# Optimization experiments

Hardware: AMD Instinct MI355X
Metric: run time of the kernel (lower is better)

## Reference

```python
import jax, jax.numpy as jnp
import numpy as np

NUM_USER = 50000
NUM_ITEM = 50000
N = NUM_USER + NUM_ITEM
DIM_FEAT = 128
DIM_LATENT = 64
DIM_ID = 64
E = 2_000_000
NUM_LAYER = 3
NEG_SLOPE = 0.01  # torch leaky_relu default


def _xavier(key, shape):
    fan_out, fan_in = shape[0], shape[1]
    std = np.sqrt(2.0 / (fan_in + fan_out)).astype(np.float32)
    return jax.random.normal(key, shape, dtype=jnp.float32) * std


def setup_inputs() -> dict:
    key = jax.random.key(0)
    ks = jax.random.split(key, 40)
    features = jax.random.normal(ks[0], (NUM_ITEM, DIM_FEAT), dtype=jnp.float32)
    edge_index = jax.random.randint(ks[1], (2, E), 0, N, dtype=jnp.int32)
    preference = _xavier(ks[2], (NUM_USER, DIM_LATENT))
    mlp_w = _xavier(ks[3], (DIM_LATENT, DIM_FEAT))
    mlp_b = jnp.zeros((DIM_LATENT,), jnp.float32)
    conv_in = [DIM_LATENT, DIM_ID, DIM_ID, DIM_ID, DIM_ID]
    lin_in = [DIM_LATENT, DIM_ID, DIM_ID, DIM_ID, DIM_ID]
    conv_w, lin_w, lin_b, g_w, g_b = [], [], [], [], []
    for i in range(5):
        conv_w.append(_xavier(ks[4 + i], (conv_in[i], DIM_ID)))        # BaseModel weight [in,out]
        lin_w.append(_xavier(ks[9 + i], (DIM_ID, lin_in[i])))           # nn.Linear weight [out,in]
        lin_b.append(jnp.zeros((DIM_ID,), jnp.float32))
        g_w.append(_xavier(ks[14 + i], (DIM_ID, 2 * DIM_ID)))           # concate=True -> in = 2*dim_id
        g_b.append(jnp.zeros((DIM_ID,), jnp.float32))
    return {"features": features, "edge_index": edge_index, "preference": preference,
            "mlp_w": mlp_w, "mlp_b": mlp_b, "conv_w": conv_w,
            "lin_w": lin_w, "lin_b": lin_b, "g_w": g_w, "g_b": g_b}


def reference(features, edge_index, preference, mlp_w, mlp_b, conv_w, lin_w, lin_b, g_w, g_b):
    leaky = lambda x: jax.nn.leaky_relu(x, NEG_SLOPE)
    src, dst = edge_index[0], edge_index[1]

    def conv(x, W):
        # BaseModel: transform then gather at src, scatter-add at dst (aggr='add')
        m = x @ W                                  # [N, dim_id]
        return jax.ops.segment_sum(m[src], dst, num_segments=N)

    temp = features @ mlp_w.T + mlp_b             # MLP (dim_latent branch)
    x = jnp.concatenate([preference, temp], axis=0)  # [N, dim_latent]
    x = x / jnp.maximum(jnp.linalg.norm(x, axis=1, keepdims=True), 1e-12)  # F.normalize

    for i in range(NUM_LAYER):  # layers 1..3 (num_layer=3)
        h = leaky(conv(x, conv_w[i]))
        x_hat = leaky(x @ lin_w[i].T + lin_b[i])
        x = leaky(jnp.concatenate([h, x_hat], axis=1) @ g_w[i].T + g_b[i])

    mu = leaky(conv(x, conv_w[3]))
    x_hat = leaky(x @ lin_w[3].T + lin_b[3])
    mu = jnp.concatenate([mu, x_hat], axis=1) @ g_w[3].T + g_b[3]

    logvar = leaky(conv(x, conv_w[4]))
    x_hat = leaky(x @ lin_w[4].T + lin_b[4])
    logvar = jnp.concatenate([logvar, x_hat], axis=1) @ g_w[4].T + g_b[4]
    return mu, logvar
```

## Files before the change

### kernel.cpp

```cpp
#include <hip/hip_runtime.h>
#include <hip/hip_fp16.h>

#define DEVINL __device__ __forceinline__

typedef _Float16 v4h __attribute__((ext_vector_type(4)));
typedef float    v4f __attribute__((ext_vector_type(4)));

constexpr int NUSER = 50000;
constexpr int NITEM = 50000;
constexpr int NTOT  = 100000;
constexpr int DF    = 128;
constexpr int D     = 64;
constexpr int NE    = 2000000;
constexpr int TR    = 32;
constexpr int ROWH  = 72;
constexpr int NCHUNK = 4;
constexpr int CSPAN  = NTOT / NCHUNK;
constexpr int CCAP   = 32;
constexpr int CAP    = NCHUNK * CCAP;
constexpr int NW     = 512;
constexpr int NPW    = 196;
constexpr int WCAP   = 4608;
constexpr int PBLK   = 512;
constexpr int EPB    = (NE + PBLK - 1) / PBLK;
constexpr int EPT    = (EPB + 255) / 256;

DEVINL float leaky(float v) { return v > 0.f ? v : 0.01f * v; }

DEVINL float2 h2f2(unsigned u) {
  __half2 h = *reinterpret_cast<__half2*>(&u);
  return __half22float2(h);
}

__global__ __launch_bounds__(256) void k_zero(int* __restrict__ p, int n) {
  int i = blockIdx.x * blockDim.x + threadIdx.x;
  if (i < n) p[i] = 0;
}

__global__ __launch_bounds__(256) void k_init_user(
    const float* __restrict__ pref, __half* __restrict__ x16) {
  int wid  = (blockIdx.x * blockDim.x + threadIdx.x) >> 6;
  int lane = threadIdx.x & 63;
  if (wid >= NUSER) return;
  float v = pref[(size_t)wid * D + lane];
  float ss = v * v;
#pragma unroll
  for (int o = 32; o; o >>= 1) ss += __shfl_xor(ss, o);
  float inv = 1.0f / fmaxf(sqrtf(ss), 1e-12f);
  x16[(size_t)wid * D + lane] = __float2half(v * inv);
}

__global__ __launch_bounds__(512) void k_init_item(
    const float* __restrict__ feat, const float* __restrict__ mlp_w,
    const float* __restrict__ mlp_b, __half* __restrict__ x16) {
  __shared__ float sF[TR * DF];
  __shared__ float sP[2][TR][D];
  int tid  = threadIdx.x;
  int lane = tid & 63;
  int wv   = tid >> 6;
  int kh   = wv & 1;
  int rg   = wv >> 1;
  float wh[D];
  const float4* wp = (const float4*)(mlp_w + (size_t)lane * DF + kh * D);
#pragma unroll
  for (int k = 0; k < D / 4; ++k) {
    float4 t = wp[k];
    wh[4 * k] = t.x; wh[4 * k + 1] = t.y; wh[4 * k + 2] = t.z; wh[4 * k + 3] = t.w;
  }
  float bias = mlp_b[lane];
  int t = blockIdx.x;
  {
    const float4* base = (const float4*)(feat + (size_t)t * TR * DF);
    float4* dstl = (float4*)sF;
#pragma unroll
    for (int s = 0; s < 2; ++s) {
      int slot = tid + s * 512;
      int gr = t * TR + (slot >> 5);
      float4 v = make_float4(0.f, 0.f, 0.f, 0.f);
      if (gr < NITEM) v = base[slot];
      dstl[slot] = v;
    }
  }
  __syncthreads();
#pragma unroll
  for (int rr = 0; rr < 8; ++rr) {
    int r = rg * 8 + rr;
    const float4* fr = (const float4*)&sF[r * DF + kh * D];
    float acc = 0.f;
#pragma unroll
    for (int k = 0; k < D / 4; ++k) {
      float4 a = fr[k];
      acc += a.x * wh[4 * k] + a.y * wh[4 * k + 1] + a.z * wh[4 * k + 2] + a.w * wh[4 * k + 3];
    }
    sP[kh][r][lane] = acc;
  }
  __syncthreads();
#pragma unroll
  for (int rr = 0; rr < 4; ++rr) {
    int r = wv * 4 + rr;
    int gr = t * TR + r;
    float v = sP[0][r][lane] + sP[1][r][lane] + bias;
    float ss = v * v;
#pragma unroll
    for (int o = 32; o; o >>= 1) ss += __shfl_xor(ss, o);
    float inv = 1.0f / fmaxf(sqrtf(ss), 1e-12f);
    if (gr < NITEM) x16[(size_t)(NUSER + gr) * D + lane] = __float2half(v * inv);
  }
}

__global__ __launch_bounds__(256) void k_part(
    const int* __restrict__ src, const int* __restrict__ dst,
    int* __restrict__ wcur, unsigned* __restrict__ part) {
  __shared__ int hcnt[NW];
  __shared__ int sc[NW];
  __shared__ int gbase[NW];
  __shared__ int hcur[NW];
  __shared__ unsigned buf[EPB];
  int tid = threadIdx.x;
  int e0 = blockIdx.x * EPB, e1 = min(NE, e0 + EPB);
  for (int i = tid; i < NW; i += 256) { hcnt[i] = 0; hcur[i] = 0; }
  __syncthreads();
  unsigned ent[EPT];
  int wid[EPT];
#pragma unroll
  for (int i = 0; i < EPT; ++i) {
    int e = e0 + tid + i * 256;
    int w = -1; unsigned v = 0;
    if (e < e1) {
      int d = dst[e];
      int s = src[e];
      w = d / NPW;
      v = ((unsigned)(d - w * NPW) << 17) | (unsigned)s;
      atomicAdd(&hcnt[w], 1);
    }
    ent[i] = v; wid[i] = w;
  }
  __syncthreads();
  {
    int i0 = tid, i1 = tid + 256;
    sc[i0] = hcnt[i0]; sc[i1] = hcnt[i1];
    __syncthreads();
    for (int o = 1; o < NW; o <<= 1) {
      int v0 = (i0 >= o) ? sc[i0 - o] : 0;
      int v1 = (i1 >= o) ? sc[i1 - o] : 0;
      __syncthreads();
      sc[i0] += v0; sc[i1] += v1;
      __syncthreads();
    }
  }
  for (int i = tid; i < NW; i += 256)
    gbase[i] = atomicAdd(&wcur[i], hcnt[i]);
  __syncthreads();
#pragma unroll
  for (int i = 0; i < EPT; ++i) {
    int w = wid[i];
    if (w >= 0) {
      int idx = atomicAdd(&hcur[w], 1);
      buf[sc[w] - hcnt[w] + idx] = ent[i];
    }
  }
  __syncthreads();
  int wvv = tid >> 6, lane = tid & 63;
  for (int b = wvv; b < NW; b += 4) {
    int len = hcnt[b];
    int lb = sc[b] - len;
    int gb = gbase[b];
    unsigned* out = part + (size_t)b * WCAP;
    for (int i = lane; i < len; i += 64)
      if (gb + i < WCAP) out[gb + i] = buf[lb + i];
  }
}

__global__ __launch_bounds__(256) void k_scatter_lds(
    const unsigned* __restrict__ part, const int* __restrict__ wcur,
    int* __restrict__ cursor, unsigned short* __restrict__ csr) {
  __shared__ unsigned short lbuck[NPW * CAP];
  __shared__ int lcur[NPW * NCHUNK];
  int tid = threadIdx.x;
  int w   = blockIdx.x;
  int nlo = w * NPW;
  int nn  = min(NPW, NTOT - nlo);
  if (nn <= 0) return;
  for (int i = tid; i < NPW * NCHUNK; i += 256) lcur[i] = 0;
  __syncthreads();
  int cnt = min(wcur[w], WCAP);
  const unsigned* basep = part + (size_t)w * WCAP;
  for (int e = tid; e < cnt; e += 256) {
    unsigned v = basep[e];
    int dl = (int)(v >> 17);
    int s  = (int)(v & 0x1ffffu);
    int c  = s / CSPAN;
    int p  = atomicAdd(&lcur[dl * NCHUNK + c], 1);
    if (p < CCAP) lbuck[dl * CAP + c * CCAP + p] = (unsigned short)(s - c * CSPAN);
  }
  __syncthreads();
  unsigned* gcsr = (unsigned*)(csr + (size_t)nlo * CAP);
  const unsigned* lsrc = (const unsigned*)lbuck;
  int words = nn * (CAP / 2);
  for (int i = tid; i < words; i += 256) gcsr[i] = lsrc[i];
  int* gcur = cursor + (size_t)nlo * NCHUNK;
  for (int i = tid; i < nn * NCHUNK; i += 256) gcur[i] = lcur[i];
}

__global__ __launch_bounds__(256) void k_agg(
    const __half* __restrict__ x16, const int* __restrict__ cnt,
    const unsigned short* __restrict__ csr, __half* __restrict__ agg16) {
  int wid  = (blockIdx.x * blockDim.x + threadIdx.x) >> 6;
  int lane = threadIdx.x & 63;
  if (wid >= NTOT) return;
  int g = lane >> 3;
  int q = lane & 7;
  int4 c4 = *(const int4*)(cnt + ((size_t)wid << 2));
  unsigned w = ((const unsigned*)(csr + (size_t)wid * CAP))[lane];
  float a[8] = {0.f, 0.f, 0.f, 0.f, 0.f, 0.f, 0.f, 0.f};
#pragma unroll
  for (int c = 0; c < NCHUNK; ++c) {
    int deg = min(c == 0 ? c4.x : c == 1 ? c4.y : c == 2 ? c4.z : c4.w, CCAP);
    int base = c * CSPAN;
    int e = 0;
    for (; e + 8 <= deg; e += 8) {
      unsigned u = __shfl(w, c * 16 + ((e + g) >> 1));
      int s = base + (int)((u >> (((e + g) & 1) * 16)) & 0xffffu);
      uint4 v = ((const uint4*)(x16 + (size_t)s * D))[q];
      float2 t;
      t = h2f2(v.x); a[0] += t.x; a[1] += t.y;
      t = h2f2(v.y); a[2] += t.x; a[3] += t.y;
      t = h2f2(v.z); a[4] += t.x; a[5] += t.y;
      t = h2f2(v.w); a[6] += t.x; a[7] += t.y;
    }
    int rem = deg - e;
    if (rem > 0) {
      unsigned u = __shfl(w, c * 16 + ((e + g) >> 1));
      if (g < rem) {
        int s = base + (int)((u >> (((e + g) & 1) * 16)) & 0xffffu);
        uint4 v = ((const uint4*)(x16 + (size_t)s * D))[q];
        float2 t;
        t = h2f2(v.x); a[0] += t.x; a[1] += t.y;
        t = h2f2(v.y); a[2] += t.x; a[3] += t.y;
        t = h2f2(v.z); a[4] += t.x; a[5] += t.y;
        t = h2f2(v.w); a[6] += t.x; a[7] += t.y;
      }
    }
  }
#pragma unroll
  for (int o = 8; o <= 32; o <<= 1) {
#pragma unroll
    for (int i = 0; i < 8; ++i) a[i] += __shfl_xor(a[i], o);
  }
  if (lane < 8) {
    __half2 h0 = __floats2half2_rn(a[0], a[1]);
    __half2 h1 = __floats2half2_rn(a[2], a[3]);
    __half2 h2 = __floats2half2_rn(a[4], a[5]);
    __half2 h3 = __floats2half2_rn(a[6], a[7]);
    uint4 out;
    out.x = *reinterpret_cast<unsigned*>(&h0);
    out.y = *reinterpret_cast<unsigned*>(&h1);
    out.z = *reinterpret_cast<unsigned*>(&h2);
    out.w = *reinterpret_cast<unsigned*>(&h3);
    ((uint4*)(agg16 + (size_t)wid * D))[q] = out;
  }
}

__global__ __launch_bounds__(256) void k_layer(
    const __half* __restrict__ aggIn, const __half* __restrict__ xIn,
    const float* __restrict__ convw, const float* __restrict__ linw,
    const float* __restrict__ linb, const float* __restrict__ gw,
    const float* __restrict__ gb,
    __half* __restrict__ out16, float* __restrict__ outf, int do_leaky) {
  __shared__ __half sA[2][TR * ROWH];
  __shared__ __half sX[2][TR * ROWH];
  __shared__ __half sH[TR * ROWH];
  __shared__ __half sXH[TR * ROWH];
  int tid  = threadIdx.x;
  int lane = tid & 63;
  int wv   = tid >> 6;
  int r    = lane & 15;
  int g    = lane >> 4;
  int nt   = wv;

  v4h Bc[4], Bl[4], Bg1[4], Bg2[4];
#pragma unroll
  for (int ks = 0; ks < 4; ++ks) {
    v4h b;
#pragma unroll
    for (int j = 0; j < 4; ++j)
      b[j] = (_Float16)convw[(16 * ks + 4 * g + j) * D + 16 * nt + r];
    Bc[ks] = b;
    const float4 tl = *(const float4*)(linw + (size_t)(16 * nt + r) * D + 16 * ks + 4 * g);
    v4h bb; bb[0] = (_Float16)tl.x; bb[1] = (_Float16)tl.y;
    bb[2] = (_Float16)tl.z; bb[3] = (_Float16)tl.w;
    Bl[ks] = bb;
    const float4 t1 = *(const float4*)(gw + (size_t)(16 * nt + r) * 2 * D + 16 * ks + 4 * g);
    v4h b1; b1[0] = (_Float16)t1.x; b1[1] = (_Float16)t1.y;
    b1[2] = (_Float16)t1.z; b1[3] = (_Float16)t1.w;
    Bg1[ks] = b1;
    const float4 t2 = *(const float4*)(gw + (size_t)(16 * nt + r) * 2 * D + D + 16 * ks + 4 * g);
    v4h b2; b2[0] = (_Float16)t2.x; b2[1] = (_Float16)t2.y;
    b2[2] = (_Float16)t2.z; b2[3] = (_Float16)t2.w;
    Bg2[ks] = b2;
  }
  float bl = linb[16 * nt + r];
  float bg = gb[16 * nt + r];

  const int ntile = NTOT / TR;
  int srow = tid >> 3;
  int scol = (tid & 7) * 8;
  uint4 pA, pX;
  int t = blockIdx.x;
  pA = ((const uint4*)(aggIn + (size_t)t * TR * D))[tid];
  pX = ((const uint4*)(xIn + (size_t)t * TR * D))[tid];
  *(uint4*)&sA[0][srow * ROWH + scol] = pA;
  *(uint4*)&sX[0][srow * ROWH + scol] = pX;
  __syncthreads();
  int buf = 0;
  for (; t < ntile; t += gridDim.x) {
    int tn = t + gridDim.x;
    if (tn < ntile) {
      pA = ((const uint4*)(aggIn + (size_t)tn * TR * D))[tid];
      pX = ((const uint4*)(xIn + (size_t)tn * TR * D))[tid];
    }
#pragma unroll
    for (int mt = 0; mt < 2; ++mt) {
      v4f ah = {0.f, 0.f, 0.f, 0.f};
      v4f ax = {bl, bl, bl, bl};
#pragma unroll
      for (int ks = 0; ks < 4; ++ks) {
        v4h aAgg = __builtin_bit_cast(v4h,
            *(const unsigned long long*)&sA[buf][(16 * mt + r) * ROWH + 16 * ks + 4 * g]);
        v4h aXf = __builtin_bit_cast(v4h,
            *(const unsigned long long*)&sX[buf][(16 * mt + r) * ROWH + 16 * ks + 4 * g]);
        ah = __builtin_amdgcn_mfma_f32_16x16x16f16(aAgg, Bc[ks], ah, 0, 0, 0);
        ax = __builtin_amdgcn_mfma_f32_16x16x16f16(aXf, Bl[ks], ax, 0, 0, 0);
      }
#pragma unroll
      for (int j = 0; j < 4; ++j) {
        sH[(16 * mt + 4 * g + j) * ROWH + 16 * nt + r]  = __float2half(leaky(ah[j]));
        sXH[(16 * mt + 4 * g + j) * ROWH + 16 * nt + r] = __float2half(leaky(ax[j]));
      }
    }
    __syncthreads();
    if (tn < ntile) {
      *(uint4*)&sA[buf ^ 1][srow * ROWH + scol] = pA;
      *(uint4*)&sX[buf ^ 1][srow * ROWH + scol] = pX;
    }
#pragma unroll
    for (int mt = 0; mt < 2; ++mt) {
      v4f ag = {bg, bg, bg, bg};
#pragma unroll
      for (int ks = 0; ks < 4; ++ks) {
        v4h fh = __builtin_bit_cast(v4h,
            *(const unsigned long long*)&sH[(16 * mt + r) * ROWH + 16 * ks + 4 * g]);
        ag = __builtin_amdgcn_mfma_f32_16x16x16f16(fh, Bg1[ks], ag, 0, 0, 0);
      }
#pragma unroll
      for (int ks = 0; ks < 4; ++ks) {
        v4h fx = __builtin_bit_cast(v4h,
            *(const unsigned long long*)&sXH[(16 * mt + r) * ROWH + 16 * ks + 4 * g]);
        ag = __builtin_amdgcn_mfma_f32_16x16x16f16(fx, Bg2[ks], ag, 0, 0, 0);
      }
#pragma unroll
      for (int j = 0; j < 4; ++j) {
        float o = ag[j];
        if (do_leaky) o = leaky(o);
        size_t gi = ((size_t)t * TR + 16 * mt + 4 * g + j) * D + 16 * nt + r;
        if (out16) out16[gi] = __float2half(o);
        else       outf[gi] = o;
      }
    }
    __syncthreads();
    buf ^= 1;
  }
}

extern "C" void kernel_launch(void* const* d_in, const int* in_sizes, int n_in,
                              void* d_out, int out_size, void* d_ws, size_t ws_size,
                              hipStream_t stream) {
  const float* features = (const float*)d_in[0];
  const int*   ei       = (const int*)d_in[1];
  const float* pref     = (const float*)d_in[2];
  const float* mlp_w    = (const float*)d_in[3];
  const float* mlp_b    = (const float*)d_in[4];
  const float* conv_w[5]; const float* lin_w[5]; const float* lin_b[5];
  const float* g_w[5];    const float* g_b[5];
  if (n_in >= 30) {
    for (int i = 0; i < 5; ++i) {
      conv_w[i] = (const float*)d_in[5 + i];
      lin_w[i]  = (const float*)d_in[10 + i];
      lin_b[i]  = (const float*)d_in[15 + i];
      g_w[i]    = (const float*)d_in[20 + i];
      g_b[i]    = (const float*)d_in[25 + i];
    }
  } else {
    const float* cw = (const float*)d_in[5];
    const float* lw = (const float*)d_in[6];
    const float* lb = (const float*)d_in[7];
    const float* gw = (const float*)d_in[8];
    const float* gb = (const float*)d_in[9];
    for (int i = 0; i < 5; ++i) {
      conv_w[i] = cw + (size_t)i * D * D;
      lin_w[i]  = lw + (size_t)i * D * D;
      lin_b[i]  = lb + (size_t)i * D;
      g_w[i]    = gw + (size_t)i * D * 2 * D;
      g_b[i]    = gb + (size_t)i * D;
    }
  }
  const int* e_src = ei;
  const int* e_dst = ei + NE;

  char* p = (char*)d_ws;
  __half* x16a  = (__half*)p; p += (size_t)NTOT * D * 2;
  __half* x16b  = (__half*)p; p += (size_t)NTOT * D * 2;
  __half* agg16 = (__half*)p; p += (size_t)NTOT * D * 2;
  __half* h16   = (__half*)p; p += (size_t)NTOT * D * 2;
  __half* xh16  = (__half*)p; p += (size_t)NTOT * D * 2;
  unsigned short* csr = (unsigned short*)p; p += (size_t)NTOT * CAP * 2;
  int*   cursor = (int*)p;   p += (size_t)NTOT * NCHUNK * 4;
  int*   wcur   = (int*)p;   p += (NW + 64) * 4;
  unsigned* part = (unsigned*)h16;
  (void)xh16;

  float* mu     = (float*)d_out;
  float* logvar = (float*)d_out + (size_t)NTOT * D;

  const int WPB = 4;
  int grid_rows  = (NTOT + WPB - 1) / WPB;
  int grid_dense = 1024;
  int ntile_item = (NITEM + TR - 1) / TR;

  k_init_user<<<(NUSER + 3) / 4, 256, 0, stream>>>(pref, x16a);
  k_init_item<<<ntile_item, 512, 0, stream>>>(features, mlp_w, mlp_b, x16a);

  k_zero<<<(NW + 255) / 256, 256, 0, stream>>>(wcur, NW);
  k_part<<<PBLK, 256, 0, stream>>>(e_src, e_dst, wcur, part);
  k_scatter_lds<<<NW, 256, 0, stream>>>(part, wcur, cursor, csr);

  __half* xa = x16a;
  __half* xb = x16b;
  for (int i = 0; i < 3; ++i) {
    k_agg<<<grid_rows, 256, 0, stream>>>(xa, cursor, csr, agg16);
    k_layer<<<grid_dense, 256, 0, stream>>>(agg16, xa, conv_w[i], lin_w[i], lin_b[i],
                                            g_w[i], g_b[i], xb, nullptr, 1);
    __half* t = xa; xa = xb; xb = t;
  }

  k_agg<<<grid_rows, 256, 0, stream>>>(xa, cursor, csr, agg16);
  k_layer<<<grid_dense, 256, 0, stream>>>(agg16, xa, conv_w[3], lin_w[3], lin_b[3],
                                          g_w[3], g_b[3], nullptr, mu, 0);
  k_layer<<<grid_dense, 256, 0, stream>>>(agg16, xa, conv_w[4], lin_w[4], lin_b[4],
                                          g_w[4], g_b[4], nullptr, logvar, 0);
}
```

Baseline: 376.6 us.

## Fold wcur zeroing into init kernel, use wave-shuffle scan, retune grid sizes

Removes the separate k_zero launch by having block 0 of k_init_user clear the wcur counters. Replaces the barrier-heavy LDS Hillis-Steele prefix scan in k_part with a wave-level shuffle scan plus a small cross-wave combine. Also doubles the partition block count, halving edges per block, and raises the dense layer grid from 1024 to 1563 blocks. Together these trim launch overhead and synchronisation, at the cost of more global atomics on wcur from the extra partition blocks.

```diff
diff --git a/kernel.cpp b/kernel.cpp
--- a/kernel.cpp
+++ b/kernel.cpp
@@ -21,7 +21,7 @@
 constexpr int NW     = 512;
 constexpr int NPW    = 196;
 constexpr int WCAP   = 4608;
-constexpr int PBLK   = 512;
+constexpr int PBLK   = 1024;
 constexpr int EPB    = (NE + PBLK - 1) / PBLK;
 constexpr int EPT    = (EPB + 255) / 256;
 
@@ -32,13 +32,12 @@
   return __half22float2(h);
 }
 
-__global__ __launch_bounds__(256) void k_zero(int* __restrict__ p, int n) {
-  int i = blockIdx.x * blockDim.x + threadIdx.x;
-  if (i < n) p[i] = 0;
-}
-
 __global__ __launch_bounds__(256) void k_init_user(
-    const float* __restrict__ pref, __half* __restrict__ x16) {
+    const float* __restrict__ pref, __half* __restrict__ x16,
+    int* __restrict__ wcur) {
+  if (blockIdx.x == 0) {
+    for (int i = threadIdx.x; i < NW + 64; i += 256) wcur[i] = 0;
+  }
   int wid  = (blockIdx.x * blockDim.x + threadIdx.x) >> 6;
   int lane = threadIdx.x & 63;
   if (wid >= NUSER) return;
@@ -115,8 +114,10 @@
   __shared__ int sc[NW];
   __shared__ int gbase[NW];
   __shared__ int hcur[NW];
+  __shared__ int wtot[4];
   __shared__ unsigned buf[EPB];
   int tid = threadIdx.x;
+  int wvv = tid >> 6, lane = tid & 63;
   int e0 = blockIdx.x * EPB, e1 = min(NE, e0 + EPB);
   for (int i = tid; i < NW; i += 256) { hcnt[i] = 0; hcur[i] = 0; }
   __syncthreads();
@@ -136,18 +137,21 @@
     ent[i] = v; wid[i] = w;
   }
   __syncthreads();
-  {
-    int i0 = tid, i1 = tid + 256;
-    sc[i0] = hcnt[i0]; sc[i1] = hcnt[i1];
-    __syncthreads();
-    for (int o = 1; o < NW; o <<= 1) {
-      int v0 = (i0 >= o) ? sc[i0 - o] : 0;
-      int v1 = (i1 >= o) ? sc[i1 - o] : 0;
-      __syncthreads();
-      sc[i0] += v0; sc[i1] += v1;
-      __syncthreads();
-    }
-  }
+  int b0 = 128 * wvv + 2 * lane;
+  int s0 = hcnt[b0], s1 = hcnt[b0 + 1];
+  int pair = s0 + s1;
+#pragma unroll
+  for (int o = 1; o < 64; o <<= 1) {
+    int t = __shfl_up(pair, o);
+    if (lane >= o) pair += t;
+  }
+  if (lane == 63) wtot[wvv] = pair;
+  __syncthreads();
+  int prefix = 0;
+#pragma unroll
+  for (int v = 0; v < 4; ++v) prefix += (v < wvv) ? wtot[v] : 0;
+  sc[b0]     = prefix + pair - s1;
+  sc[b0 + 1] = prefix + pair;
   for (int i = tid; i < NW; i += 256)
     gbase[i] = atomicAdd(&wcur[i], hcnt[i]);
   __syncthreads();
@@ -160,7 +164,6 @@
     }
   }
   __syncthreads();
-  int wvv = tid >> 6, lane = tid & 63;
   for (int b = wvv; b < NW; b += 4) {
     int len = hcnt[b];
     int lb = sc[b] - len;
@@ -424,13 +427,12 @@
 
   const int WPB = 4;
   int grid_rows  = (NTOT + WPB - 1) / WPB;
-  int grid_dense = 1024;
+  int grid_dense = 1563;
   int ntile_item = (NITEM + TR - 1) / TR;
 
-  k_init_user<<<(NUSER + 3) / 4, 256, 0, stream>>>(pref, x16a);
+  k_init_user<<<(NUSER + 3) / 4, 256, 0, stream>>>(pref, x16a, wcur);
   k_init_item<<<ntile_item, 512, 0, stream>>>(features, mlp_w, mlp_b, x16a);
 
-  k_zero<<<(NW + 255) / 256, 256, 0, stream>>>(wcur, NW);
   k_part<<<PBLK, 256, 0, stream>>>(e_src, e_dst, wcur, part);
   k_scatter_lds<<<NW, 256, 0, stream>>>(part, wcur, cursor, csr);
 
```

Result: slower. 402.7 us (+6.9%).
